# Optimization experiments

Measured on AMD Instinct MI355X. Metric: run time of the kernel, lower is better.

Reference implementation:

```python
import jax, jax.numpy as jnp
import numpy as np

D_MODEL, D_STATE, D_CONV, D_INNER, DT_RANK = 1024, 16, 4, 2048, 64
B_SZ, L = 4, 2048

def setup_inputs() -> dict:
    key = jax.random.key(0)
    ks = jax.random.split(key, 7)
    return {
        "hidden_states": jax.random.normal(ks[0], (B_SZ, L, D_MODEL), jnp.float32),
        "in_proj_w": jax.random.normal(ks[1], (2 * D_INNER, D_MODEL), jnp.float32) * (D_MODEL ** -0.5),
        "conv_w": jax.random.normal(ks[2], (D_INNER, 1, D_CONV), jnp.float32) * 0.5,
        "conv_b": jax.random.normal(ks[3], (D_INNER,), jnp.float32) * 0.1,
        "x_proj_w": jax.random.normal(ks[4], (DT_RANK + 2 * D_STATE, D_INNER), jnp.float32) * (D_INNER ** -0.5),
        "dt_proj_w": jax.random.normal(ks[5], (D_INNER, DT_RANK), jnp.float32) * (DT_RANK ** -0.5),
        "A_log": jax.random.uniform(ks[6], (D_INNER, D_STATE), jnp.float32, 0.0, 2.0),
    }

def reference(hidden_states, in_proj_w, conv_w, conv_b, x_proj_w, dt_proj_w, A_log):
    b, l, d = hidden_states.shape
    # in_proj: (b,l,d) x (2*d_inner,d)^T -> (b, 2*d_inner, l)
    xz = jnp.einsum('bld,ed->bel', hidden_states, in_proj_w)
    x, z = jnp.split(xz, 2, axis=1)  # each (b, d_inner, l); z unused downstream
    A = -jnp.exp(A_log)              # (d_inner, d_state)
    # causal depthwise conv1d (left pad d_conv-1) + SiLU
    x = jax.lax.conv_general_dilated(
        x, conv_w, window_strides=(1,), padding=[(D_CONV - 1, 0)],
        feature_group_count=D_INNER,
        dimension_numbers=('NCH', 'OIH', 'NCH'))
    x = jax.nn.silu(x + conv_b[None, :, None])  # (b, d_inner, l)
    # x_proj: (b,l,dt_rank+2*d_state)
    x_dbl = jnp.einsum('bdl,ed->ble', x, x_proj_w)
    dt, B_mat, C_mat = jnp.split(x_dbl, [DT_RANK, DT_RANK + D_STATE], axis=-1)
    dt = jnp.einsum('blr,dr->bdl', dt, dt_proj_w)          # (b, d_inner, l), no bias
    B_mat = jnp.swapaxes(B_mat, 1, 2)                      # (b, d_state, l)
    C_mat = jnp.swapaxes(C_mat, 1, 2)                      # (b, d_state, l)
    return (dt, A, B_mat, C_mat, x)
```

## Files before the change

### kernel.cpp

```cpp
#include <hip/hip_runtime.h>
#include <hip/hip_bf16.h>
#include <math.h>

#define D_MODEL 1024
#define D_STATE 16
#define D_CONV  4
#define D_INNER 2048
#define DT_RANK 64
#define B_SZ    4
#define L_SEQ   2048

#define OFF_DT 0
#define OFF_A  (B_SZ * D_INNER * L_SEQ)
#define OFF_B  (OFF_A + D_INNER * D_STATE)
#define OFF_C  (OFF_B + B_SZ * D_STATE * L_SEQ)
#define OFF_X  (OFF_C + B_SZ * D_STATE * L_SEQ)

typedef __attribute__((ext_vector_type(8))) short bf16x8;
typedef __attribute__((ext_vector_type(8))) unsigned short us8;
typedef __attribute__((ext_vector_type(4))) float f32x4;
typedef unsigned short ushort_t;
typedef unsigned int uint_t;

static __device__ __forceinline__ ushort_t f2bf(float f) {
  __hip_bfloat16 h = __float2bfloat16(f);
  return *(ushort_t*)&h;
}
static __device__ __forceinline__ float bf2f(ushort_t u) {
  union { uint_t u; float f; } c;
  c.u = ((uint_t)u) << 16;
  return c.f;
}

#define N4_HS   (B_SZ * L_SEQ * D_MODEL / 4)
#define N4_W    (D_INNER * D_MODEL / 4)
#define N4_XW   ((DT_RANK + 2 * D_STATE) * D_INNER / 4)
#define N4_DW   (D_INNER * DT_RANK / 4)
#define N4_Z0   (B_SZ * DT_RANK * L_SEQ / 4)
#define N4_Z1   (2 * B_SZ * D_STATE * L_SEQ / 4)
#define N4_A    (D_INNER * D_STATE / 4)
#define N4_TOT  (N4_HS + N4_W + N4_XW + N4_DW + N4_Z0 + N4_Z1 + N4_A)

__global__ __launch_bounds__(256) void k_prep(
    const float4* __restrict__ hs, const float4* __restrict__ ipw,
    const float4* __restrict__ xpw, const float4* __restrict__ dpw,
    const float4* __restrict__ alog,
    ushort4* __restrict__ bfHS, ushort4* __restrict__ bfW,
    ushort4* __restrict__ xwb, ushort4* __restrict__ dwb,
    float4* __restrict__ z0, float4* __restrict__ z1,
    float4* __restrict__ aout) {
  int i = blockIdx.x * 256 + threadIdx.x;
  if (i < N4_HS) {
    float4 v = hs[i];
    ushort4 o; o.x = f2bf(v.x); o.y = f2bf(v.y); o.z = f2bf(v.z); o.w = f2bf(v.w);
    bfHS[i] = o;
    return;
  }
  i -= N4_HS;
  if (i < N4_W) {
    float4 v = ipw[i];
    ushort4 o; o.x = f2bf(v.x); o.y = f2bf(v.y); o.z = f2bf(v.z); o.w = f2bf(v.w);
    bfW[i] = o;
    return;
  }
  i -= N4_W;
  if (i < N4_XW) {
    float4 v = xpw[i];
    ushort4 o; o.x = f2bf(v.x); o.y = f2bf(v.y); o.z = f2bf(v.z); o.w = f2bf(v.w);
    xwb[i] = o;
    return;
  }
  i -= N4_XW;
  if (i < N4_DW) {
    float4 v = dpw[i];
    ushort4 o; o.x = f2bf(v.x); o.y = f2bf(v.y); o.z = f2bf(v.z); o.w = f2bf(v.w);
    dwb[i] = o;
    return;
  }
  i -= N4_DW;
  if (i < N4_Z0) { z0[i] = (float4){0.f, 0.f, 0.f, 0.f}; return; }
  i -= N4_Z0;
  if (i < N4_Z1) { z1[i] = (float4){0.f, 0.f, 0.f, 0.f}; return; }
  i -= N4_Z1;
  if (i < N4_A) {
    float4 v = alog[i];
    float4 o;
    o.x = -expf(v.x); o.y = -expf(v.y); o.z = -expf(v.z); o.w = -expf(v.w);
    aout[i] = o;
  }
}

__global__ __launch_bounds__(256) void k_inproj_mfma(
    const ushort_t* __restrict__ Wb,
    const ushort_t* __restrict__ HSb,
    ushort_t* __restrict__ Cout) {
  const int flat = blockIdx.x + 16 * blockIdx.y + 256 * blockIdx.z;
  const int swz  = (flat & 7) * 128 + (flat >> 3);
  const int bn = swz & 15;
  const int bm = (swz >> 4) & 15;
  const int b  = swz >> 8;

  __shared__ ushort_t As[128 * 32];
  __shared__ ushort_t Bs[128 * 32];
  const int tid  = threadIdx.x;
  const int wv   = tid >> 6;
  const int lane = tid & 63;
  const int wr = wv >> 1, wc = wv & 1;

  const int srow = tid >> 2;
  const int ss   = tid & 3;

  const ushort_t* Ag = Wb + (size_t)(bm * 128) * D_MODEL;
  const ushort_t* Bg = HSb + (size_t)b * L_SEQ * D_MODEL
                           + (size_t)(bn * 128) * D_MODEL;

  f32x4 acc[4][4];
#pragma unroll
  for (int i = 0; i < 4; ++i)
#pragma unroll
    for (int j = 0; j < 4; ++j) acc[i][j] = (f32x4){0.f, 0.f, 0.f, 0.f};

  const int ksel = lane >> 4;
  const int frow = lane & 15;

  for (int k0 = 0; k0 < D_MODEL; k0 += 32) {
#pragma unroll
    for (int q = 0; q < 2; ++q) {
      int row = q * 64 + srow;
      int xs  = ss ^ ((row >> 1) & 3);
      const ushort_t* ga = Ag + (size_t)row * D_MODEL + k0 + xs * 8;
      const ushort_t* gb = Bg + (size_t)row * D_MODEL + k0 + xs * 8;
      ushort_t* la = As + (q * 256 + wv * 64) * 8;
      ushort_t* lb = Bs + (q * 256 + wv * 64) * 8;
      __builtin_amdgcn_global_load_lds((const __attribute__((address_space(1))) void*)ga,
                                       (__attribute__((address_space(3))) void*)la, 16, 0, 0);
      __builtin_amdgcn_global_load_lds((const __attribute__((address_space(1))) void*)gb,
                                       (__attribute__((address_space(3))) void*)lb, 16, 0, 0);
    }
    __syncthreads();

    bf16x8 af[4], bfr[4];
#pragma unroll
    for (int m = 0; m < 4; ++m) {
      int row = wr * 64 + m * 16 + frow;
      af[m] = *(const bf16x8*)(As + (row * 4 + (ksel ^ ((row >> 1) & 3))) * 8);
    }
#pragma unroll
    for (int n = 0; n < 4; ++n) {
      int row = wc * 64 + n * 16 + frow;
      bfr[n] = *(const bf16x8*)(Bs + (row * 4 + (ksel ^ ((row >> 1) & 3))) * 8);
    }
#pragma unroll
    for (int m = 0; m < 4; ++m)
#pragma unroll
      for (int n = 0; n < 4; ++n)
        acc[m][n] = __builtin_amdgcn_mfma_f32_16x16x32_bf16(af[m], bfr[n], acc[m][n], 0, 0, 0);
    __syncthreads();
  }

  const int crow0 = (lane >> 4) * 4;
  const int ccol  = lane & 15;
  ushort_t* Cb = Cout + (size_t)b * D_INNER * L_SEQ;
#pragma unroll
  for (int m = 0; m < 4; ++m) {
    int gr0 = bm * 128 + wr * 64 + m * 16 + crow0;
#pragma unroll
    for (int n = 0; n < 4; ++n) {
      int gc = bn * 128 + wc * 64 + n * 16 + ccol;
#pragma unroll
      for (int i = 0; i < 4; ++i)
        Cb[(size_t)(gr0 + i) * L_SEQ + gc] = f2bf(acc[m][n][i]);
    }
  }
}

__global__ __launch_bounds__(256) void k_xproj_fused(
    const ushort_t* __restrict__ XWb,
    const ushort_t* __restrict__ Xpre,
    const float* __restrict__ CW,
    const float* __restrict__ CB,
    float* __restrict__ Xout,
    float* __restrict__ XDBL,
    float* __restrict__ OutB,
    float* __restrict__ OutC) {
  const int ln = blockIdx.x;
  const int sk = blockIdx.y;
  const int b  = blockIdx.z;
  __shared__ ushort_t As[96 * 40];
  __shared__ ushort_t Bs[128 * 34];
  const int tid  = threadIdx.x;
  const int wv   = tid >> 6;
  const int lane = tid & 63;
  const int wr = wv >> 1, wc = wv & 1;
  const int ksel = lane >> 4;
  const int frow = lane & 15;

  f32x4 acc[3][4];
#pragma unroll
  for (int i = 0; i < 3; ++i)
#pragma unroll
    for (int j = 0; j < 4; ++j) acc[i][j] = (f32x4){0.f, 0.f, 0.f, 0.f};

  for (int k0 = 0; k0 < 256; k0 += 32) {
    const int koff = sk * 256 + k0;
    {
      int row = tid >> 2, s = tid & 3;
      bf16x8 v = *(const bf16x8*)(XWb + (size_t)row * D_INNER + koff + s * 8);
      *(bf16x8*)(As + row * 40 + s * 8) = v;
      if (tid < 128) {
        int row2 = 64 + (tid >> 2);
        bf16x8 v2 = *(const bf16x8*)(XWb + (size_t)row2 * D_INNER + koff + s * 8);
        *(bf16x8*)(As + row2 * 40 + s * 8) = v2;
      }
    }
#pragma unroll
    for (int j = 0; j < 2; ++j) {
      int u = tid + 256 * j;
      int n4 = u & 31;
      int kp = u >> 5;
      int l0 = ln * 128 + 4 * n4;
      float sv[2][4];
#pragma unroll
      for (int r = 0; r < 2; ++r) {
        int d = koff + 2 * kp + r;
        const ushort_t* row = Xpre + ((size_t)b * D_INNER + d) * L_SEQ;
        ushort4 cur = *(const ushort4*)(row + l0);
        float em3 = 0.f, em2 = 0.f, em1 = 0.f;
        if (l0 >= 4) {
          ushort4 pv = *(const ushort4*)(row + l0 - 4);
          em3 = bf2f(pv.y); em2 = bf2f(pv.z); em1 = bf2f(pv.w);
        }
        float ee[7] = {em3, em2, em1, bf2f(cur.x), bf2f(cur.y), bf2f(cur.z), bf2f(cur.w)};
        float4 w = *(const float4*)(CW + d * 4);
        float bias = CB[d];
#pragma unroll
        for (int i = 0; i < 4; ++i) {
          float v = w.x * ee[i] + w.y * ee[i + 1] + w.z * ee[i + 2] + w.w * ee[i + 3] + bias;
          sv[r][i] = v / (1.f + expf(-v));
        }
        *(float4*)(Xout + ((size_t)b * D_INNER + d) * L_SEQ + l0) =
            make_float4(sv[r][0], sv[r][1], sv[r][2], sv[r][3]);
      }
#pragma unroll
      for (int i = 0; i < 4; ++i) {
        uint_t pk = (uint_t)f2bf(sv[0][i]) | ((uint_t)f2bf(sv[1][i]) << 16);
        *(uint_t*)(Bs + (4 * n4 + i) * 34 + 2 * kp) = pk;
      }
    }
    __syncthreads();

    bf16x8 af[3], bfr[4];
#pragma unroll
    for (int mi = 0; mi < 3; ++mi) {
      int row = wr * 48 + mi * 16 + frow;
      af[mi] = *(const bf16x8*)(As + row * 40 + ksel * 8);
    }
#pragma unroll
    for (int ni = 0; ni < 4; ++ni) {
      int n = wc * 64 + ni * 16 + frow;
      const uint_t* p = (const uint_t*)(Bs + n * 34);
      union { uint_t u[4]; bf16x8 v; } fr;
#pragma unroll
      for (int q = 0; q < 4; ++q) fr.u[q] = p[ksel * 4 + q];
      bfr[ni] = fr.v;
    }
#pragma unroll
    for (int mi = 0; mi < 3; ++mi)
#pragma unroll
      for (int ni = 0; ni < 4; ++ni)
        acc[mi][ni] = __builtin_amdgcn_mfma_f32_16x16x32_bf16(af[mi], bfr[ni], acc[mi][ni], 0, 0, 0);
    __syncthreads();
  }

  const int crow0 = (lane >> 4) * 4;
  const int ccol  = lane & 15;
#pragma unroll
  for (int mi = 0; mi < 3; ++mi) {
    int e0 = wr * 48 + mi * 16 + crow0;
    float* base;
    int eoff;
    if (e0 < 64)      { base = XDBL + (size_t)b * 64 * L_SEQ; eoff = e0; }
    else if (e0 < 80) { base = OutB + (size_t)b * D_STATE * L_SEQ; eoff = e0 - 64; }
    else              { base = OutC + (size_t)b * D_STATE * L_SEQ; eoff = e0 - 80; }
#pragma unroll
    for (int ni = 0; ni < 4; ++ni) {
      int l = ln * 128 + wc * 64 + ni * 16 + ccol;
#pragma unroll
      for (int r = 0; r < 4; ++r)
        atomicAdd(base + (size_t)(eoff + r) * L_SEQ + l, acc[mi][ni][r]);
    }
  }
}

__global__ __launch_bounds__(256) void k_dt_mfma(
    const ushort_t* __restrict__ DWb,
    const float* __restrict__ XDBL,
    float* __restrict__ DT) {
  const int ln = blockIdx.x;
  const int dm = blockIdx.y;
  const int b  = blockIdx.z;
  __shared__ ushort_t As[128 * 72];
  __shared__ ushort_t Bs[128 * 68];
  const int tid  = threadIdx.x;
  const int wv   = tid >> 6;
  const int lane = tid & 63;
  const int wr = wv >> 1, wc = wv & 1;
  const int ksel = lane >> 4;
  const int frow = lane & 15;

#pragma unroll
  for (int q = 0; q < 4; ++q) {
    int u = tid + 256 * q;
    int row = u >> 3, s = u & 7;
    *(bf16x8*)(As + row * 72 + s * 8) =
        *(const bf16x8*)(DWb + (size_t)(dm * 128 + row) * DT_RANK + s * 8);
  }
#pragma unroll
  for (int q = 0; q < 4; ++q) {
    int u = tid + 256 * q;
    int n4 = u & 31;
    int kp = u >> 5;
    const float* g = XDBL + ((size_t)b * DT_RANK + 2 * kp) * L_SEQ + ln * 128 + 4 * n4;
    float4 x0 = *(const float4*)g;
    float4 x1 = *(const float4*)(g + L_SEQ);
    float e0[4] = {x0.x, x0.y, x0.z, x0.w};
    float e1[4] = {x1.x, x1.y, x1.z, x1.w};
#pragma unroll
    for (int i = 0; i < 4; ++i) {
      uint_t pk = (uint_t)f2bf(e0[i]) | ((uint_t)f2bf(e1[i]) << 16);
      *(uint_t*)(Bs + (4 * n4 + i) * 68 + 2 * kp) = pk;
    }
  }
  __syncthreads();

  f32x4 acc[4][4];
#pragma unroll
  for (int i = 0; i < 4; ++i)
#pragma unroll
    for (int j = 0; j < 4; ++j) acc[i][j] = (f32x4){0.f, 0.f, 0.f, 0.f};

#pragma unroll
  for (int ks = 0; ks < 2; ++ks) {
    bf16x8 af[4], bfr[4];
#pragma unroll
    for (int m = 0; m < 4; ++m) {
      int row = wr * 64 + m * 16 + frow;
      af[m] = *(const bf16x8*)(As + row * 72 + ks * 32 + ksel * 8);
    }
#pragma unroll
    for (int n = 0; n < 4; ++n) {
      int nn = wc * 64 + n * 16 + frow;
      bfr[n] = *(const bf16x8*)(Bs + nn * 68 + ks * 32 + ksel * 8);
    }
#pragma unroll
    for (int m = 0; m < 4; ++m)
#pragma unroll
      for (int n = 0; n < 4; ++n)
        acc[m][n] = __builtin_amdgcn_mfma_f32_16x16x32_bf16(af[m], bfr[n], acc[m][n], 0, 0, 0);
  }

  const int crow0 = (lane >> 4) * 4;
  const int ccol  = lane & 15;
  float* Cb = DT + (size_t)b * D_INNER * L_SEQ;
#pragma unroll
  for (int m = 0; m < 4; ++m) {
    int gr0 = dm * 128 + wr * 64 + m * 16 + crow0;
#pragma unroll
    for (int n = 0; n < 4; ++n) {
      int gc = ln * 128 + wc * 64 + n * 16 + ccol;
#pragma unroll
      for (int i = 0; i < 4; ++i)
        Cb[(size_t)(gr0 + i) * L_SEQ + gc] = acc[m][n][i];
    }
  }
}

extern "C" void kernel_launch(void* const* d_in, const int* in_sizes, int n_in,
                              void* d_out, int out_size, void* d_ws, size_t ws_size,
                              hipStream_t stream) {
  const float* hs   = (const float*)d_in[0];
  const float* ipw  = (const float*)d_in[1];
  const float* cw   = (const float*)d_in[2];
  const float* cb   = (const float*)d_in[3];
  const float* xpw  = (const float*)d_in[4];
  const float* dpw  = (const float*)d_in[5];
  const float* alog = (const float*)d_in[6];

  float* out    = (float*)d_out;
  float* dt_out = out + OFF_DT;
  float* a_out  = out + OFF_A;
  float* b_out  = out + OFF_B;
  float* c_out  = out + OFF_C;
  float* x_out  = out + OFF_X;

  unsigned short* bfHS = (unsigned short*)x_out;
  unsigned short* bfW  = bfHS + (size_t)B_SZ * L_SEQ * D_MODEL;
  unsigned short* xpre = (unsigned short*)dt_out;
  float* xdbl = (float*)d_ws;
  unsigned short* xwb = (unsigned short*)((char*)d_ws + 2097152);
  unsigned short* dwb = (unsigned short*)((char*)d_ws + 2097152 + 393216);

  k_prep<<<dim3((N4_TOT + 255) / 256), 256, 0, stream>>>(
      (const float4*)hs, (const float4*)ipw, (const float4*)xpw,
      (const float4*)dpw, (const float4*)alog,
      (ushort4*)bfHS, (ushort4*)bfW, (ushort4*)xwb, (ushort4*)dwb,
      (float4*)xdbl, (float4*)b_out, (float4*)a_out);

  k_inproj_mfma<<<dim3(16, 16, 4), 256, 0, stream>>>(bfW, bfHS, xpre);
  k_xproj_fused<<<dim3(16, 8, 4), 256, 0, stream>>>(xwb, xpre, cw, cb,
                                                    x_out, xdbl, b_out, c_out);
  k_dt_mfma<<<dim3(16, 16, 4), 256, 0, stream>>>(dwb, xdbl, dt_out);
}
```

Measured before the change: 133.0 us.

## Widen in_proj GEMM tile to 128x256 and use 32x32x16 MFMA

```diff
diff --git a/kernel.cpp b/kernel.cpp
--- a/kernel.cpp
+++ b/kernel.cpp
@@ -19,6 +19,7 @@
 typedef __attribute__((ext_vector_type(8))) short bf16x8;
 typedef __attribute__((ext_vector_type(8))) unsigned short us8;
 typedef __attribute__((ext_vector_type(4))) float f32x4;
+typedef __attribute__((ext_vector_type(16))) float f32x16;
 typedef unsigned short ushort_t;
 typedef unsigned int uint_t;
 
@@ -94,82 +95,90 @@
     const ushort_t* __restrict__ Wb,
     const ushort_t* __restrict__ HSb,
     ushort_t* __restrict__ Cout) {
-  const int flat = blockIdx.x + 16 * blockIdx.y + 256 * blockIdx.z;
-  const int swz  = (flat & 7) * 128 + (flat >> 3);
-  const int bn = swz & 15;
-  const int bm = (swz >> 4) & 15;
-  const int b  = swz >> 8;
+  const int flat = blockIdx.x + 8 * blockIdx.y + 128 * blockIdx.z;
+  const int swz  = (flat & 7) * 64 + (flat >> 3);
+  const int bn = swz & 7;
+  const int bm = (swz >> 3) & 15;
+  const int b  = swz >> 7;
 
   __shared__ ushort_t As[128 * 32];
-  __shared__ ushort_t Bs[128 * 32];
+  __shared__ ushort_t Bs[256 * 32];
   const int tid  = threadIdx.x;
   const int wv   = tid >> 6;
   const int lane = tid & 63;
-  const int wr = wv >> 1, wc = wv & 1;
-
-  const int srow = tid >> 2;
-  const int ss   = tid & 3;
+  const int l31  = lane & 31;
+  const int lhi  = lane >> 5;
 
   const ushort_t* Ag = Wb + (size_t)(bm * 128) * D_MODEL;
   const ushort_t* Bg = HSb + (size_t)b * L_SEQ * D_MODEL
-                           + (size_t)(bn * 128) * D_MODEL;
-
-  f32x4 acc[4][4];
-#pragma unroll
-  for (int i = 0; i < 4; ++i)
-#pragma unroll
-    for (int j = 0; j < 4; ++j) acc[i][j] = (f32x4){0.f, 0.f, 0.f, 0.f};
-
-  const int ksel = lane >> 4;
-  const int frow = lane & 15;
+                           + (size_t)(bn * 256) * D_MODEL;
+
+  f32x16 acc[4][2];
+#pragma unroll
+  for (int m = 0; m < 4; ++m)
+#pragma unroll
+    for (int n = 0; n < 2; ++n)
+#pragma unroll
+      for (int r = 0; r < 16; ++r) acc[m][n][r] = 0.f;
 
   for (int k0 = 0; k0 < D_MODEL; k0 += 32) {
 #pragma unroll
     for (int q = 0; q < 2; ++q) {
-      int row = q * 64 + srow;
-      int xs  = ss ^ ((row >> 1) & 3);
+      int slot = q * 256 + tid;
+      int row = slot >> 2, s = slot & 3;
+      int xs = s ^ ((row >> 1) & 3);
       const ushort_t* ga = Ag + (size_t)row * D_MODEL + k0 + xs * 8;
-      const ushort_t* gb = Bg + (size_t)row * D_MODEL + k0 + xs * 8;
       ushort_t* la = As + (q * 256 + wv * 64) * 8;
-      ushort_t* lb = Bs + (q * 256 + wv * 64) * 8;
       __builtin_amdgcn_global_load_lds((const __attribute__((address_space(1))) void*)ga,
                                        (__attribute__((address_space(3))) void*)la, 16, 0, 0);
+    }
+#pragma unroll
+    for (int q = 0; q < 4; ++q) {
+      int slot = q * 256 + tid;
+      int row = slot >> 2, s = slot & 3;
+      int xs = s ^ ((row >> 1) & 3);
+      const ushort_t* gb = Bg + (size_t)row * D_MODEL + k0 + xs * 8;
+      ushort_t* lb = Bs + (q * 256 + wv * 64) * 8;
       __builtin_amdgcn_global_load_lds((const __attribute__((address_space(1))) void*)gb,
                                        (__attribute__((address_space(3))) void*)lb, 16, 0, 0);
     }
     __syncthreads();
 
-    bf16x8 af[4], bfr[4];
-#pragma unroll
-    for (int m = 0; m < 4; ++m) {
-      int row = wr * 64 + m * 16 + frow;
-      af[m] = *(const bf16x8*)(As + (row * 4 + (ksel ^ ((row >> 1) & 3))) * 8);
-    }
-#pragma unroll
-    for (int n = 0; n < 4; ++n) {
-      int row = wc * 64 + n * 16 + frow;
-      bfr[n] = *(const bf16x8*)(Bs + (row * 4 + (ksel ^ ((row >> 1) & 3))) * 8);
-    }
-#pragma unroll
-    for (int m = 0; m < 4; ++m)
-#pragma unroll
-      for (int n = 0; n < 4; ++n)
-        acc[m][n] = __builtin_amdgcn_mfma_f32_16x16x32_bf16(af[m], bfr[n], acc[m][n], 0, 0, 0);
+#pragma unroll
+    for (int ks = 0; ks < 2; ++ks) {
+      bf16x8 af[4], bfr[2];
+#pragma unroll
+      for (int m = 0; m < 4; ++m) {
+        int row = m * 32 + l31;
+        int xs = (ks * 2 + lhi) ^ ((row >> 1) & 3);
+        af[m] = *(const bf16x8*)(As + (row * 4 + xs) * 8);
+      }
+#pragma unroll
+      for (int n = 0; n < 2; ++n) {
+        int row = wv * 64 + n * 32 + l31;
+        int xs = (ks * 2 + lhi) ^ ((row >> 1) & 3);
+        bfr[n] = *(const bf16x8*)(Bs + (row * 4 + xs) * 8);
+      }
+#pragma unroll
+      for (int m = 0; m < 4; ++m)
+#pragma unroll
+        for (int n = 0; n < 2; ++n)
+          acc[m][n] = __builtin_amdgcn_mfma_f32_32x32x16_bf16(af[m], bfr[n], acc[m][n], 0, 0, 0);
+    }
     __syncthreads();
   }
 
-  const int crow0 = (lane >> 4) * 4;
-  const int ccol  = lane & 15;
   ushort_t* Cb = Cout + (size_t)b * D_INNER * L_SEQ;
 #pragma unroll
   for (int m = 0; m < 4; ++m) {
-    int gr0 = bm * 128 + wr * 64 + m * 16 + crow0;
-#pragma unroll
-    for (int n = 0; n < 4; ++n) {
-      int gc = bn * 128 + wc * 64 + n * 16 + ccol;
-#pragma unroll
-      for (int i = 0; i < 4; ++i)
-        Cb[(size_t)(gr0 + i) * L_SEQ + gc] = f2bf(acc[m][n][i]);
+#pragma unroll
+    for (int n = 0; n < 2; ++n) {
+      int gc = bn * 256 + wv * 64 + n * 32 + l31;
+#pragma unroll
+      for (int reg = 0; reg < 16; ++reg) {
+        int gr = bm * 128 + m * 32 + (reg & 3) + 8 * (reg >> 2) + 4 * lhi;
+        Cb[(size_t)gr * L_SEQ + gc] = f2bf(acc[m][n][reg]);
+      }
     }
   }
 }
@@ -406,7 +415,7 @@
       (ushort4*)bfHS, (ushort4*)bfW, (ushort4*)xwb, (ushort4*)dwb,
       (float4*)xdbl, (float4*)b_out, (float4*)a_out);
 
-  k_inproj_mfma<<<dim3(16, 16, 4), 256, 0, stream>>>(bfW, bfHS, xpre);
+  k_inproj_mfma<<<dim3(8, 16, 4), 256, 0, stream>>>(bfW, bfHS, xpre);
   k_xproj_fused<<<dim3(16, 8, 4), 256, 0, stream>>>(xwb, xpre, cw, cb,
                                                     x_out, xdbl, b_out, c_out);
   k_dt_mfma<<<dim3(16, 16, 4), 256, 0, stream>>>(dwb, xdbl, dt_out);
```

Result: slower. 155.7 us (+17.1%).
